# Kernel tuning notes

Hardware: AMD Instinct MI355X
Metric: run time of the kernel (lower is better)

The kernel has to match this reference:

```python
import jax, jax.numpy as jnp
import numpy as np

NUM_HEADS = 16
HEAD_DIM = 128
Q_SCALE = 0.05
Q_ZP = 8.0


def _quant_dequant_int4(x, scale, zp):
    # simulate int4 pack/unpack: q = clamp(round(x/scale + zp), 0, 15); deq = (q - zp) * scale
    qv = jnp.clip(jnp.round(x / scale + zp), 0.0, 15.0)
    return (qv - zp) * scale


def setup_inputs() -> dict:
    key = jax.random.key(0)
    kq, kk, kv = jax.random.split(key, 3)
    B, Sq, Sk, D = 4, 2048, 2048, 2048
    q = jax.random.normal(kq, (B, Sq, D), dtype=jnp.float32)
    k = jax.random.normal(kk, (B, Sk, D), dtype=jnp.float32)
    v = jax.random.normal(kv, (B, Sk, D), dtype=jnp.float32)
    mask = jnp.ones((B, Sk), dtype=bool)
    return {"q": q, "k": k, "v": v, "mask": mask, "q_start": 1000000000}


def reference(q, k, v, mask, q_start):
    B, Sq, d_model = q.shape
    Sk = k.shape[1]
    H, Dh = NUM_HEADS, HEAD_DIM
    # [B, H, S, Dh]
    qh = q.reshape(B, Sq, H, Dh).transpose(0, 2, 1, 3)
    kh = k.reshape(B, Sk, H, Dh).transpose(0, 2, 1, 3)
    vh = v.reshape(B, Sk, H, Dh).transpose(0, 2, 1, 3)
    # int4 quant-dequant of K and V (per-tensor scale/zero-point path)
    kd = _quant_dequant_int4(kh, Q_SCALE, Q_ZP)
    vd = _quant_dequant_int4(vh, Q_SCALE, Q_ZP)
    inv_sqrt_d = 1.0 / np.sqrt(Dh).astype(np.float32)
    scores = jnp.einsum('bhmd,bhnd->bhmn', qh, kd) * inv_sqrt_d  # [B,H,Sq,Sk]
    neg_inf = jnp.finfo(scores.dtype).min
    # key padding mask [B, Sk]
    scores = jnp.where(mask[:, None, None, :], scores, neg_inf)
    # causal mask with absolute query offset q_start (disabled when q_start is huge)
    m_abs = q_start + jnp.arange(Sq)[:, None]  # absolute query positions
    n_pos = jnp.arange(Sk)[None, :]
    scores = jnp.where(n_pos <= m_abs, scores, neg_inf)
    attn = jax.nn.softmax(scores, axis=-1)
    out = jnp.einsum('bhmn,bhnd->bhmd', attn, vd)  # [B,H,Sq,Dh]
    return out.transpose(0, 2, 1, 3).reshape(B, Sq, d_model)
```

## Files before the change

### kernel.cpp

```cpp
#include <hip/hip_runtime.h>


typedef __attribute__((ext_vector_type(8))) short short8;
typedef __attribute__((ext_vector_type(16))) float f32x16;

#define DEVI __device__ __forceinline__

namespace {

constexpr int DM = 2048;
constexpr int SQ = 2048;
constexpr int SK = 2048;
constexpr int DH = 128;
constexpr int KVB = 32;
constexpr int NT = SK / KVB;
constexpr int TILE_E = KVB * DH;
constexpr float CEXP = 0.12752051393f;

union US8 { unsigned short u[8]; short8 v; };
union UP4 { unsigned int u[4]; short8 v; };

DEVI unsigned short f2bf(float f) {
  unsigned int u = __float_as_uint(f);
  return (unsigned short)((u + 0x7fffu + ((u >> 16) & 1u)) >> 16);
}

DEVI float dq(float x) {
  float t = __builtin_rintf(__builtin_fmaf(x, 20.0f, 8.0f));
  t = __builtin_fmaxf(t, 0.0f);
  t = __builtin_fminf(t, 15.0f);
  return (t - 8.0f) * 0.05f;
}

DEVI unsigned short dqb(float x) { return f2bf(dq(x)); }

}

__global__ __launch_bounds__(512)
void eit3_pre(const float* __restrict__ kg, const float* __restrict__ vg,
              unsigned short* __restrict__ kws, unsigned short* __restrict__ vws)
{
  const int tid = threadIdx.x;
  const int t = blockIdx.x, h = blockIdx.y, b = blockIdx.z;
  const size_t tb = (((size_t)(b * 16 + h)) * NT + t) * TILE_E;
  __shared__ __align__(16) unsigned short KL[32 * 136];
  __shared__ __align__(16) unsigned short VL[32 * 136];

  {
    const int r = tid >> 4, c8 = (tid & 15) * 8;
    const float* ks = kg + ((size_t)b * SK + (size_t)t * KVB + r) * DM + h * DH + c8;
    const float* vs = vg + ((size_t)b * SK + (size_t)t * KVB + r) * DM + h * DH + c8;
    float4 ka = *(const float4*)ks, kb4 = *(const float4*)(ks + 4);
    float4 va = *(const float4*)vs, vb4 = *(const float4*)(vs + 4);
    US8 ok, ov;
    ok.u[0] = dqb(ka.x); ok.u[1] = dqb(ka.y); ok.u[2] = dqb(ka.z); ok.u[3] = dqb(ka.w);
    ok.u[4] = dqb(kb4.x); ok.u[5] = dqb(kb4.y); ok.u[6] = dqb(kb4.z); ok.u[7] = dqb(kb4.w);
    ov.u[0] = dqb(va.x); ov.u[1] = dqb(va.y); ov.u[2] = dqb(va.z); ov.u[3] = dqb(va.w);
    ov.u[4] = dqb(vb4.x); ov.u[5] = dqb(vb4.y); ov.u[6] = dqb(vb4.z); ov.u[7] = dqb(vb4.w);
    *(short8*)(KL + r * 136 + c8) = ok.v;
    *(short8*)(VL + r * 136 + c8) = ov.v;
  }
  __syncthreads();

  const int l = tid & 63;
  const int lq = l & 31, lh = (l >> 5) * 8;
  {
    const int s = tid >> 6;
    short8 o = *(const short8*)(KL + lq * 136 + s * 16 + lh);
    *(short8*)(kws + tb + (size_t)tid * 8) = o;
  }
  {
    const int f = tid >> 6, n = f >> 1, ks2 = f & 1;
    US8 o;
#pragma unroll
    for (int j = 0; j < 8; ++j)
      o.u[j] = VL[(ks2 * 16 + lh + j) * 136 + n * 32 + lq];
    *(short8*)(vws + tb + (size_t)tid * 8) = o.v;
  }
}

__global__ __launch_bounds__(64, 3)
void eit3_attn(const unsigned short* __restrict__ kws,
               const unsigned short* __restrict__ vws,
               const float* __restrict__ qg,
               const unsigned char* __restrict__ maskg,
               const int* __restrict__ qsg, float* __restrict__ outg)
{
  const int lane = threadIdx.x;
  const int hi   = lane >> 5;
  const int ql   = lane & 31;
  const int hi8  = hi * 8;
  const int phys = blockIdx.x;
  const int xcd = phys & 7, slot = phys >> 3;
  const int bh  = 8 * (slot >> 6) + xcd;
  const int sub = slot & 63;
  const int q0  = (sub >> 2) * 128 + (sub & 3) * 32;
  const int h = bh & 15, b = bh >> 4;
  const long long qstart = (long long)qsg[0];

  const unsigned char* mrow = maskg + (size_t)b * SK;
  int ok_u8 = 1, ok_i32 = 1;
  {
    const unsigned int* p = (const unsigned int*)(mrow + lane * 32);
#pragma unroll
    for (int j = 0; j < 8; ++j) {
      unsigned int x = p[j];
      int a = (x & 0xFFu) && (x & 0xFF00u) && (x & 0xFF0000u) && (x & 0xFF000000u);
      ok_u8 &= a;
      ok_i32 &= (x == 1u);
    }
  }
  const bool mask_all = __all(ok_u8) || __all(ok_i32);

  const size_t tbase = (size_t)bh * NT * TILE_E;
  const unsigned short* kb = kws + tbase + lane * 8;
  const unsigned short* vb = vws + tbase + lane * 8;

  short8 qf[8];
  {
    const float* qp = qg + ((size_t)b * SQ + q0 + ql) * DM + h * DH + hi8;
#pragma unroll
    for (int s = 0; s < 8; ++s) {
      float4 fa = *(const float4*)(qp + s * 16);
      float4 fb = *(const float4*)(qp + s * 16 + 4);
      US8 t;
      t.u[0] = f2bf(fa.x * CEXP); t.u[1] = f2bf(fa.y * CEXP);
      t.u[2] = f2bf(fa.z * CEXP); t.u[3] = f2bf(fa.w * CEXP);
      t.u[4] = f2bf(fb.x * CEXP); t.u[5] = f2bf(fb.y * CEXP);
      t.u[6] = f2bf(fb.z * CEXP); t.u[7] = f2bf(fb.w * CEXP);
      qf[s] = t.v;
    }
  }

  f32x16 zv;
#pragma unroll
  for (int r = 0; r < 16; ++r) zv[r] = 0.0f;
  f32x16 acc[4];
  acc[0] = zv; acc[1] = zv; acc[2] = zv; acc[3] = zv;
  float L = 0.0f;
  const long long qlim = qstart + (long long)(q0 + ql);

  for (int t = 0; t < NT; ++t) {
    const int kv0 = t * KVB;

    short8 kv[8];
    {
      const unsigned short* p = kb + (size_t)t * TILE_E;
#pragma unroll
      for (int s = 0; s < 8; ++s) kv[s] = *(const short8*)(p + s * 512);
    }

    f32x16 st = zv;
    __builtin_amdgcn_s_setprio(1);
#pragma unroll
    for (int s = 0; s < 8; ++s)
      st = __builtin_amdgcn_mfma_f32_32x32x16_bf16(kv[s], qf[s], st, 0, 0, 0);
    __builtin_amdgcn_s_setprio(0);

    {
      const unsigned short* p = vb + (size_t)t * TILE_E;
#pragma unroll
      for (int f = 0; f < 8; ++f) kv[f] = *(const short8*)(p + f * 512);
    }

    const bool fast = mask_all && ((long long)(kv0 + KVB - 1) <= qstart + (long long)q0);

    if (!fast) {
#pragma unroll
      for (int r = 0; r < 16; ++r) {
        int nl = (r & 3) + 8 * (r >> 2) + 4 * hi;
        bool ok = (mrow[kv0 + nl] != 0) && ((long long)(kv0 + nl) <= qlim);
        if (!ok) st[r] = -3.0e38f;
      }
    }

#pragma unroll
    for (int r = 0; r < 16; ++r)
      st[r] = __builtin_amdgcn_exp2f(st[r]);

    float s8[8];
#pragma unroll
    for (int i = 0; i < 8; ++i) s8[i] = st[i] + st[i + 8];
#pragma unroll
    for (int i = 0; i < 4; ++i) s8[i] = s8[i] + s8[i + 4];
    float ps = (s8[0] + s8[1]) + (s8[2] + s8[3]);
    ps += __shfl_xor(ps, 32);
    L += ps;

    short8 pa[2];
#pragma unroll
    for (int ks = 0; ks < 2; ++ks) {
      const int m8 = ks * 8;
      unsigned int X0, X1, Y0, Y1;
      asm("v_cvt_pk_bf16_f32 %0, %1, %2" : "=v"(X0) : "v"(st[m8 + 0]), "v"(st[m8 + 1]));
      asm("v_cvt_pk_bf16_f32 %0, %1, %2" : "=v"(X1) : "v"(st[m8 + 2]), "v"(st[m8 + 3]));
      asm("v_cvt_pk_bf16_f32 %0, %1, %2" : "=v"(Y0) : "v"(st[m8 + 4]), "v"(st[m8 + 5]));
      asm("v_cvt_pk_bf16_f32 %0, %1, %2" : "=v"(Y1) : "v"(st[m8 + 6]), "v"(st[m8 + 7]));
      asm("v_permlane32_swap_b32 %0, %1" : "+v"(X0), "+v"(Y0));
      asm("v_permlane32_swap_b32 %0, %1" : "+v"(X1), "+v"(Y1));
      UP4 P;
      P.u[0] = X0; P.u[1] = X1; P.u[2] = Y0; P.u[3] = Y1;
      pa[ks] = P.v;
    }

    __builtin_amdgcn_s_setprio(1);
#pragma unroll
    for (int n = 0; n < 4; ++n) {
#pragma unroll
      for (int ks = 0; ks < 2; ++ks)
        acc[n] = __builtin_amdgcn_mfma_f32_32x32x16_bf16(pa[ks], kv[n * 2 + ks],
                                                         acc[n], 0, 0, 0);
    }
    __builtin_amdgcn_s_setprio(0);
  }

  if (L == 0.0f) L = 1.0f;
  float rinv = 1.0f / L;
#pragma unroll
  for (int r = 0; r < 16; ++r) {
    int cr = (r & 3) + 8 * (r >> 2) + 4 * hi;
    float inv = __shfl(rinv, cr);
    float* op = outg + ((size_t)b * SQ + q0 + cr) * DM + h * DH + ql;
    op[0]  = acc[0][r] * inv;
    op[32] = acc[1][r] * inv;
    op[64] = acc[2][r] * inv;
    op[96] = acc[3][r] * inv;
  }
}

__global__ __launch_bounds__(512, 2)
void eit3_attn_fb(const float* __restrict__ qg, const float* __restrict__ kg,
                  const float* __restrict__ vg, const unsigned char* __restrict__ maskg,
                  const int* __restrict__ qsg, float* __restrict__ outg)
{
  const int tid  = threadIdx.x;
  const int lane = tid & 63;
  const int w    = tid >> 6;
  const int hi   = lane >> 5;
  const int ql   = lane & 31;
  const int qb = blockIdx.x;
  const int h  = blockIdx.y;
  const int b  = blockIdx.z;
  const int q0 = qb * 256;
  const long long qstart = (long long)qsg[0];

  __shared__ __align__(16) unsigned short Ksh[64 * 128];
  __shared__ __align__(16) unsigned short Vsh[64 * 128];
  __shared__ unsigned char mskSh[64];

  const unsigned int vbase = (unsigned int)(size_t)(void*)Vsh;

  const unsigned char* mrow = maskg + (size_t)b * SK;
  int ok_u8, ok_i32;
  {
    const unsigned char* p4 = mrow + tid * 4;
    unsigned char b0 = p4[0], b1 = p4[1], b2 = p4[2], b3 = p4[3];
    ok_u8  = (b0 && b1 && b2 && b3);
    ok_i32 = (b0 && !b1 && !b2 && !b3);
  }
  const int a_u8  = __syncthreads_and(ok_u8);
  const int a_i32 = __syncthreads_and(ok_i32);
  const bool mask_all = (a_u8 | a_i32) != 0;

  short8 qf[8];
  {
    const int qrow = q0 + w * 32 + ql;
    const float* qp = qg + ((size_t)b * SQ + qrow) * DM + h * DH + hi * 8;
#pragma unroll
    for (int s = 0; s < 8; ++s) {
      float4 fa = *(const float4*)(qp + s * 16);
      float4 fb = *(const float4*)(qp + s * 16 + 4);
      US8 t;
      t.u[0] = f2bf(fa.x); t.u[1] = f2bf(fa.y); t.u[2] = f2bf(fa.z); t.u[3] = f2bf(fa.w);
      t.u[4] = f2bf(fb.x); t.u[5] = f2bf(fb.y); t.u[6] = f2bf(fb.z); t.u[7] = f2bf(fb.w);
      qf[s] = t.v;
    }
  }

  f32x16 zv;
#pragma unroll
  for (int r = 0; r < 16; ++r) zv[r] = 0.0f;
  f32x16 acc[4];
  acc[0] = zv; acc[1] = zv; acc[2] = zv; acc[3] = zv;
  float M = -3.0e38f, L = 0.0f;

  const float* kptr = kg + ((size_t)b * SK) * DM + h * DH;
  const float* vptr = vg + ((size_t)b * SK) * DM + h * DH;

  constexpr float CEXP2 = 0.12752051393f;
  for (int kv0 = 0; kv0 < SK; kv0 += 64) {
    __syncthreads();
#pragma unroll
    for (int j = 0; j < 2; ++j) {
      int idx = tid + 512 * j;
      int n = idx >> 4, d8 = idx & 15;
      const float* gp = kptr + (size_t)(kv0 + n) * DM + d8 * 8;
      float4 fa = *(const float4*)gp;
      float4 fb = *(const float4*)(gp + 4);
      US8 t;
      t.u[0] = dqb(fa.x); t.u[1] = dqb(fa.y); t.u[2] = dqb(fa.z); t.u[3] = dqb(fa.w);
      t.u[4] = dqb(fb.x); t.u[5] = dqb(fb.y); t.u[6] = dqb(fb.z); t.u[7] = dqb(fb.w);
      int ui = (n * 128 + d8 * 8) ^ ((n & 7) << 3);
      *(short8*)(Ksh + ui) = t.v;
    }
    {
      int kr = w * 8 + (lane & 7);
      int c3 = lane >> 3;
#pragma unroll
      for (int j = 0; j < 4; ++j) {
        int d4 = c3 + 8 * j;
        const float* gp = vptr + (size_t)(kv0 + kr) * DM + d4 * 4;
        float4 fa = *(const float4*)gp;
        ushort4 tv;
        tv.x = dqb(fa.x); tv.y = dqb(fa.y); tv.z = dqb(fa.z); tv.w = dqb(fa.w);
        int d = d4 * 4;
        int ui = ((kr >> 2) * 8 + (d >> 4)) * 64 + (kr & 3) * 16 + (d & 15);
        *(ushort4*)(Vsh + ui) = tv;
      }
    }
    const bool causal_ok = ((long long)kv0 + 63) <= (qstart + (long long)q0);
    const bool fast = mask_all && causal_ok;
    if (!fast && w == 0) mskSh[lane] = mrow[kv0 + lane];
    __syncthreads();

    f32x16 st[2];
#pragma unroll
    for (int t = 0; t < 2; ++t) {
      f32x16 sa = zv;
#pragma unroll
      for (int s = 0; s < 8; ++s) {
        int kr = t * 32 + ql;
        int ui = (kr * 128 + s * 16 + hi * 8) ^ ((kr & 7) << 3);
        short8 af = *(const short8*)(Ksh + ui);
        sa = __builtin_amdgcn_mfma_f32_32x32x16_bf16(af, qf[s], sa, 0, 0, 0);
      }
      st[t] = sa;
    }
    if (!fast) {
      const long long qlim = qstart + (long long)(q0 + w * 32 + ql);
#pragma unroll
      for (int t = 0; t < 2; ++t) {
#pragma unroll
        for (int r = 0; r < 16; ++r) {
          int nl = t * 32 + (r & 3) + 8 * (r >> 2) + 4 * hi;
          bool ok = (mskSh[nl] != 0) && ((long long)(kv0 + nl) <= qlim);
          if (!ok) st[t][r] = -3.0e38f;
        }
      }
    }
    f32x16 red;
#pragma unroll
    for (int r = 0; r < 16; ++r) red[r] = __builtin_fmaxf(st[0][r], st[1][r]);
#pragma unroll
    for (int r = 0; r < 8; ++r) red[r] = __builtin_fmaxf(red[r], red[r + 8]);
#pragma unroll
    for (int r = 0; r < 4; ++r) red[r] = __builtin_fmaxf(red[r], red[r + 4]);
    float pmax = __builtin_fmaxf(__builtin_fmaxf(red[0], red[1]),
                                 __builtin_fmaxf(red[2], red[3]));
    pmax = __builtin_fmaxf(pmax, __shfl_xor(pmax, 32));
    const float Mnew = __builtin_fmaxf(M, pmax);
    const float scale = __builtin_amdgcn_exp2f((M - Mnew) * CEXP2);
#pragma unroll
    for (int t = 0; t < 2; ++t) {
#pragma unroll
      for (int r = 0; r < 16; ++r)
        st[t][r] = __builtin_amdgcn_exp2f((st[t][r] - Mnew) * CEXP2);
    }
    if (!fast) {
      const long long qlim = qstart + (long long)(q0 + w * 32 + ql);
#pragma unroll
      for (int t = 0; t < 2; ++t) {
#pragma unroll
        for (int r = 0; r < 16; ++r) {
          int nl = t * 32 + (r & 3) + 8 * (r >> 2) + 4 * hi;
          bool ok = (mskSh[nl] != 0) && ((long long)(kv0 + nl) <= qlim);
          if (!ok) st[t][r] = 0.0f;
        }
      }
    }
    f32x16 sx;
#pragma unroll
    for (int r = 0; r < 16; ++r) sx[r] = st[0][r] + st[1][r];
#pragma unroll
    for (int r = 0; r < 8; ++r) sx[r] = sx[r] + sx[r + 8];
#pragma unroll
    for (int r = 0; r < 4; ++r) sx[r] = sx[r] + sx[r + 4];
    float ps = (sx[0] + sx[1]) + (sx[2] + sx[3]);
    ps += __shfl_xor(ps, 32);
    L = L * scale + ps;
    if (!__all(Mnew == M)) {
#pragma unroll
      for (int r = 0; r < 16; ++r) {
        float sc = __shfl(scale, (r & 3) + 8 * (r >> 2) + 4 * hi);
        acc[0][r] *= sc; acc[1][r] *= sc; acc[2][r] *= sc; acc[3][r] *= sc;
      }
    }
    M = Mnew;

    short8 pa[4];
#pragma unroll
    for (int ks = 0; ks < 4; ++ks) {
      const int t = ks >> 1;
      const int m8 = (ks & 1) * 8;
      unsigned int X0, X1, Y0, Y1;
      asm("v_cvt_pk_bf16_f32 %0, %1, %2" : "=v"(X0) : "v"(st[t][m8 + 0]), "v"(st[t][m8 + 1]));
      asm("v_cvt_pk_bf16_f32 %0, %1, %2" : "=v"(X1) : "v"(st[t][m8 + 2]), "v"(st[t][m8 + 3]));
      asm("v_cvt_pk_bf16_f32 %0, %1, %2" : "=v"(Y0) : "v"(st[t][m8 + 4]), "v"(st[t][m8 + 5]));
      asm("v_cvt_pk_bf16_f32 %0, %1, %2" : "=v"(Y1) : "v"(st[t][m8 + 6]), "v"(st[t][m8 + 7]));
      asm("v_permlane32_swap_b32 %0, %1" : "+v"(X0), "+v"(Y0));
      asm("v_permlane32_swap_b32 %0, %1" : "+v"(X1), "+v"(Y1));
      UP4 P;
      P.u[0] = X0; P.u[1] = X1; P.u[2] = Y0; P.u[3] = Y1;
      pa[ks] = P.v;
    }
#pragma unroll
    for (int n = 0; n < 4; ++n) {
      unsigned long long t0[4], t1[4];
#pragma unroll
      for (int ks = 0; ks < 4; ++ks) {
        unsigned int addr = vbase
          + (unsigned int)(((4 * ks + 2 * hi) * 8 + 2 * n + ((lane >> 4) & 1)) * 128)
          + (unsigned int)((lane & 15) * 8);
        asm volatile("ds_read_b64_tr_b16 %0, %1" : "=v"(t0[ks]) : "v"(addr));
        asm volatile("ds_read_b64_tr_b16 %0, %1 offset:1024" : "=v"(t1[ks]) : "v"(addr));
      }
      asm volatile("s_waitcnt lgkmcnt(0)" ::: "memory");
      __builtin_amdgcn_sched_barrier(0);
#pragma unroll
      for (int ks = 0; ks < 4; ++ks) {
        union { unsigned long long q[2]; short8 v; } vb2;
        vb2.q[0] = t0[ks]; vb2.q[1] = t1[ks];
        acc[n] = __builtin_amdgcn_mfma_f32_32x32x16_bf16(pa[ks], vb2.v, acc[n], 0, 0, 0);
      }
    }
  }

  if (L == 0.0f) L = 1.0f;
  float rinv = 1.0f / L;
#pragma unroll
  for (int r = 0; r < 16; ++r) {
    int cr = (r & 3) + 8 * (r >> 2) + 4 * hi;
    float inv = __shfl(rinv, cr);
    float* op = outg + ((size_t)b * SQ + (q0 + w * 32 + cr)) * DM + h * DH + ql;
    op[0]  = acc[0][r] * inv;
    op[32] = acc[1][r] * inv;
    op[64] = acc[2][r] * inv;
    op[96] = acc[3][r] * inv;
  }
}

extern "C" void kernel_launch(void* const* d_in, const int* in_sizes, int n_in,
                              void* d_out, int out_size, void* d_ws, size_t ws_size,
                              hipStream_t stream) {
  (void)in_sizes; (void)n_in; (void)out_size;
  const float* q = (const float*)d_in[0];
  const float* k = (const float*)d_in[1];
  const float* v = (const float*)d_in[2];
  const unsigned char* mask = (const unsigned char*)d_in[3];
  const int* qs = (const int*)d_in[4];

  const size_t need = (size_t)2 * 16777216 * 2;
  if (ws_size >= need) {
    unsigned short* kws = (unsigned short*)d_ws;
    unsigned short* vws = kws + 16777216;
    dim3 pgrid(NT, 16, 4);
    eit3_pre<<<pgrid, dim3(512), 0, stream>>>(k, v, kws, vws);
    eit3_attn<<<dim3(4096), dim3(64), 0, stream>>>(kws, vws, q, mask, qs, (float*)d_out);
  } else {
    dim3 grid(SQ / 256, 16, 4);
    eit3_attn_fb<<<grid, dim3(512), 0, stream>>>(q, k, v, mask, qs, (float*)d_out);
  }
}
```

Before: 216.4 us.

## Process two query tiles per wave and double-buffer K/V register loads

Each single-wave block now handles 64 query rows (two 32-row tiles) instead of 32, so every K and V fragment loaded is reused for twice as many MFMAs, and the grid is halved. K/V fragments for the next tile are prefetched into a second register set while the current tile computes. This roughly doubles accumulator and fragment register use and drops the occupancy hint, which may lower waves per SIMD and reduce latency hiding.

```diff
diff --git a/kernel.cpp b/kernel.cpp
--- a/kernel.cpp
+++ b/kernel.cpp
@@ -79,7 +79,7 @@
   }
 }
 
-__global__ __launch_bounds__(64, 3)
+__global__ __launch_bounds__(64)
 void eit3_attn(const unsigned short* __restrict__ kws,
                const unsigned short* __restrict__ vws,
                const float* __restrict__ qg,
@@ -92,9 +92,8 @@
   const int hi8  = hi * 8;
   const int phys = blockIdx.x;
   const int xcd = phys & 7, slot = phys >> 3;
-  const int bh  = 8 * (slot >> 6) + xcd;
-  const int sub = slot & 63;
-  const int q0  = (sub >> 2) * 128 + (sub & 3) * 32;
+  const int bh  = 8 * (slot >> 5) + xcd;
+  const int q0  = (slot & 31) * 64;
   const int h = bh & 15, b = bh >> 4;
   const long long qstart = (long long)qsg[0];
 
@@ -116,52 +115,66 @@
   const unsigned short* kb = kws + tbase + lane * 8;
   const unsigned short* vb = vws + tbase + lane * 8;
 
-  short8 qf[8];
+  short8 qf0[8], qf1[8];
   {
     const float* qp = qg + ((size_t)b * SQ + q0 + ql) * DM + h * DH + hi8;
 #pragma unroll
     for (int s = 0; s < 8; ++s) {
-      float4 fa = *(const float4*)(qp + s * 16);
-      float4 fb = *(const float4*)(qp + s * 16 + 4);
-      US8 t;
-      t.u[0] = f2bf(fa.x * CEXP); t.u[1] = f2bf(fa.y * CEXP);
-      t.u[2] = f2bf(fa.z * CEXP); t.u[3] = f2bf(fa.w * CEXP);
-      t.u[4] = f2bf(fb.x * CEXP); t.u[5] = f2bf(fb.y * CEXP);
-      t.u[6] = f2bf(fb.z * CEXP); t.u[7] = f2bf(fb.w * CEXP);
-      qf[s] = t.v;
+      float4 a0 = *(const float4*)(qp + s * 16);
+      float4 c0 = *(const float4*)(qp + s * 16 + 4);
+      float4 a1 = *(const float4*)(qp + 32 * DM + s * 16);
+      float4 c1 = *(const float4*)(qp + 32 * DM + s * 16 + 4);
+      US8 t0, t1;
+      t0.u[0] = f2bf(a0.x * CEXP); t0.u[1] = f2bf(a0.y * CEXP);
+      t0.u[2] = f2bf(a0.z * CEXP); t0.u[3] = f2bf(a0.w * CEXP);
+      t0.u[4] = f2bf(c0.x * CEXP); t0.u[5] = f2bf(c0.y * CEXP);
+      t0.u[6] = f2bf(c0.z * CEXP); t0.u[7] = f2bf(c0.w * CEXP);
+      t1.u[0] = f2bf(a1.x * CEXP); t1.u[1] = f2bf(a1.y * CEXP);
+      t1.u[2] = f2bf(a1.z * CEXP); t1.u[3] = f2bf(a1.w * CEXP);
+      t1.u[4] = f2bf(c1.x * CEXP); t1.u[5] = f2bf(c1.y * CEXP);
+      t1.u[6] = f2bf(c1.z * CEXP); t1.u[7] = f2bf(c1.w * CEXP);
+      qf0[s] = t0.v; qf1[s] = t1.v;
     }
   }
 
   f32x16 zv;
 #pragma unroll
   for (int r = 0; r < 16; ++r) zv[r] = 0.0f;
-  f32x16 acc[4];
-  acc[0] = zv; acc[1] = zv; acc[2] = zv; acc[3] = zv;
-  float L = 0.0f;
-  const long long qlim = qstart + (long long)(q0 + ql);
-
-  for (int t = 0; t < NT; ++t) {
+  f32x16 acc0[4], acc1[4];
+#pragma unroll
+  for (int n = 0; n < 4; ++n) { acc0[n] = zv; acc1[n] = zv; }
+  float L0 = 0.0f, L1 = 0.0f;
+  const long long qlim0 = qstart + (long long)(q0 + ql);
+
+  short8 kfA[8], vfA[8], kfB[8], vfB[8];
+  {
+#pragma unroll
+    for (int s = 0; s < 8; ++s) kfA[s] = *(const short8*)(kb + s * 512);
+#pragma unroll
+    for (int s = 0; s < 8; ++s) vfA[s] = *(const short8*)(vb + s * 512);
+  }
+
+  auto step = [&](int t, short8 (&kfP)[8], short8 (&vfP)[8],
+                  short8 (&kfN)[8], short8 (&vfN)[8]) {
     const int kv0 = t * KVB;
-
-    short8 kv[8];
     {
-      const unsigned short* p = kb + (size_t)t * TILE_E;
-#pragma unroll
-      for (int s = 0; s < 8; ++s) kv[s] = *(const short8*)(p + s * 512);
-    }
-
-    f32x16 st = zv;
+      const int tn = (t + 1 < NT) ? (t + 1) : (NT - 1);
+      const unsigned short* pk = kb + (size_t)tn * TILE_E;
+      const unsigned short* pv = vb + (size_t)tn * TILE_E;
+#pragma unroll
+      for (int s = 0; s < 8; ++s) kfN[s] = *(const short8*)(pk + s * 512);
+#pragma unroll
+      for (int s = 0; s < 8; ++s) vfN[s] = *(const short8*)(pv + s * 512);
+    }
+
+    f32x16 st0 = zv, st1 = zv;
     __builtin_amdgcn_s_setprio(1);
 #pragma unroll
-    for (int s = 0; s < 8; ++s)
-      st = __builtin_amdgcn_mfma_f32_32x32x16_bf16(kv[s], qf[s], st, 0, 0, 0);
+    for (int s = 0; s < 8; ++s) {
+      st0 = __builtin_amdgcn_mfma_f32_32x32x16_bf16(kfP[s], qf0[s], st0, 0, 0, 0);
+      st1 = __builtin_amdgcn_mfma_f32_32x32x16_bf16(kfP[s], qf1[s], st1, 0, 0, 0);
+    }
     __builtin_amdgcn_s_setprio(0);
-
-    {
-      const unsigned short* p = vb + (size_t)t * TILE_E;
-#pragma unroll
-      for (int f = 0; f < 8; ++f) kv[f] = *(const short8*)(p + f * 512);
-    }
 
     const bool fast = mask_all && ((long long)(kv0 + KVB - 1) <= qstart + (long long)q0);
 
@@ -169,62 +182,88 @@
 #pragma unroll
       for (int r = 0; r < 16; ++r) {
         int nl = (r & 3) + 8 * (r >> 2) + 4 * hi;
-        bool ok = (mrow[kv0 + nl] != 0) && ((long long)(kv0 + nl) <= qlim);
-        if (!ok) st[r] = -3.0e38f;
-      }
-    }
-
-#pragma unroll
-    for (int r = 0; r < 16; ++r)
-      st[r] = __builtin_amdgcn_exp2f(st[r]);
-
-    float s8[8];
-#pragma unroll
-    for (int i = 0; i < 8; ++i) s8[i] = st[i] + st[i + 8];
-#pragma unroll
-    for (int i = 0; i < 4; ++i) s8[i] = s8[i] + s8[i + 4];
-    float ps = (s8[0] + s8[1]) + (s8[2] + s8[3]);
-    ps += __shfl_xor(ps, 32);
-    L += ps;
-
-    short8 pa[2];
-#pragma unroll
-    for (int ks = 0; ks < 2; ++ks) {
-      const int m8 = ks * 8;
-      unsigned int X0, X1, Y0, Y1;
-      asm("v_cvt_pk_bf16_f32 %0, %1, %2" : "=v"(X0) : "v"(st[m8 + 0]), "v"(st[m8 + 1]));
-      asm("v_cvt_pk_bf16_f32 %0, %1, %2" : "=v"(X1) : "v"(st[m8 + 2]), "v"(st[m8 + 3]));
-      asm("v_cvt_pk_bf16_f32 %0, %1, %2" : "=v"(Y0) : "v"(st[m8 + 4]), "v"(st[m8 + 5]));
-      asm("v_cvt_pk_bf16_f32 %0, %1, %2" : "=v"(Y1) : "v"(st[m8 + 6]), "v"(st[m8 + 7]));
-      asm("v_permlane32_swap_b32 %0, %1" : "+v"(X0), "+v"(Y0));
-      asm("v_permlane32_swap_b32 %0, %1" : "+v"(X1), "+v"(Y1));
-      UP4 P;
-      P.u[0] = X0; P.u[1] = X1; P.u[2] = Y0; P.u[3] = Y1;
-      pa[ks] = P.v;
+        bool okm = (mrow[kv0 + nl] != 0);
+        bool ok0 = okm && ((long long)(kv0 + nl) <= qlim0);
+        bool ok1 = okm && ((long long)(kv0 + nl) <= qlim0 + 32);
+        if (!ok0) st0[r] = -3.0e38f;
+        if (!ok1) st1[r] = -3.0e38f;
+      }
+    }
+
+#pragma unroll
+    for (int r = 0; r < 16; ++r) {
+      st0[r] = __builtin_amdgcn_exp2f(st0[r]);
+      st1[r] = __builtin_amdgcn_exp2f(st1[r]);
+    }
+
+    float s80[8], s81[8];
+#pragma unroll
+    for (int i = 0; i < 8; ++i) { s80[i] = st0[i] + st0[i + 8]; s81[i] = st1[i] + st1[i + 8]; }
+#pragma unroll
+    for (int i = 0; i < 4; ++i) { s80[i] = s80[i] + s80[i + 4]; s81[i] = s81[i] + s81[i + 4]; }
+    float p0 = (s80[0] + s80[1]) + (s80[2] + s80[3]);
+    float p1 = (s81[0] + s81[1]) + (s81[2] + s81[3]);
+    p0 += __shfl_xor(p0, 32);
+    p1 += __shfl_xor(p1, 32);
+    L0 += p0; L1 += p1;
+
+    short8 pa0[2], pa1[2];
+#pragma unroll
+    for (int half = 0; half < 2; ++half) {
+      const f32x16& sth = half ? st1 : st0;
+      short8* pah = half ? pa1 : pa0;
+#pragma unroll
+      for (int ks = 0; ks < 2; ++ks) {
+        const int m8 = ks * 8;
+        unsigned int X0, X1, Y0, Y1;
+        asm("v_cvt_pk_bf16_f32 %0, %1, %2" : "=v"(X0) : "v"(sth[m8 + 0]), "v"(sth[m8 + 1]));
+        asm("v_cvt_pk_bf16_f32 %0, %1, %2" : "=v"(X1) : "v"(sth[m8 + 2]), "v"(sth[m8 + 3]));
+        asm("v_cvt_pk_bf16_f32 %0, %1, %2" : "=v"(Y0) : "v"(sth[m8 + 4]), "v"(sth[m8 + 5]));
+        asm("v_cvt_pk_bf16_f32 %0, %1, %2" : "=v"(Y1) : "v"(sth[m8 + 6]), "v"(sth[m8 + 7]));
+        asm("v_permlane32_swap_b32 %0, %1" : "+v"(X0), "+v"(Y0));
+        asm("v_permlane32_swap_b32 %0, %1" : "+v"(X1), "+v"(Y1));
+        UP4 P;
+        P.u[0] = X0; P.u[1] = X1; P.u[2] = Y0; P.u[3] = Y1;
+        pah[ks] = P.v;
+      }
     }
 
     __builtin_amdgcn_s_setprio(1);
 #pragma unroll
     for (int n = 0; n < 4; ++n) {
 #pragma unroll
-      for (int ks = 0; ks < 2; ++ks)
-        acc[n] = __builtin_amdgcn_mfma_f32_32x32x16_bf16(pa[ks], kv[n * 2 + ks],
-                                                         acc[n], 0, 0, 0);
+      for (int ks = 0; ks < 2; ++ks) {
+        acc0[n] = __builtin_amdgcn_mfma_f32_32x32x16_bf16(pa0[ks], vfP[n * 2 + ks],
+                                                          acc0[n], 0, 0, 0);
+        acc1[n] = __builtin_amdgcn_mfma_f32_32x32x16_bf16(pa1[ks], vfP[n * 2 + ks],
+                                                          acc1[n], 0, 0, 0);
+      }
     }
     __builtin_amdgcn_s_setprio(0);
-  }
-
-  if (L == 0.0f) L = 1.0f;
-  float rinv = 1.0f / L;
+  };
+
+  for (int t = 0; t < NT; t += 2) {
+    step(t,     kfA, vfA, kfB, vfB);
+    step(t + 1, kfB, vfB, kfA, vfA);
+  }
+
+  if (L0 == 0.0f) L0 = 1.0f;
+  if (L1 == 0.0f) L1 = 1.0f;
+  float ri0 = 1.0f / L0, ri1 = 1.0f / L1;
 #pragma unroll
   for (int r = 0; r < 16; ++r) {
     int cr = (r & 3) + 8 * (r >> 2) + 4 * hi;
-    float inv = __shfl(rinv, cr);
-    float* op = outg + ((size_t)b * SQ + q0 + cr) * DM + h * DH + ql;
-    op[0]  = acc[0][r] * inv;
-    op[32] = acc[1][r] * inv;
-    op[64] = acc[2][r] * inv;
-    op[96] = acc[3][r] * inv;
+    float i0 = __shfl(ri0, cr), i1 = __shfl(ri1, cr);
+    float* op0 = outg + ((size_t)b * SQ + q0 + cr) * DM + h * DH + ql;
+    float* op1 = op0 + 32 * DM;
+    op0[0]  = acc0[0][r] * i0;
+    op0[32] = acc0[1][r] * i0;
+    op0[64] = acc0[2][r] * i0;
+    op0[96] = acc0[3][r] * i0;
+    op1[0]  = acc1[0][r] * i1;
+    op1[32] = acc1[1][r] * i1;
+    op1[64] = acc1[2][r] * i1;
+    op1[96] = acc1[3][r] * i1;
   }
 }
 
@@ -465,7 +504,7 @@
     unsigned short* vws = kws + 16777216;
     dim3 pgrid(NT, 16, 4);
     eit3_pre<<<pgrid, dim3(512), 0, stream>>>(k, v, kws, vws);
-    eit3_attn<<<dim3(4096), dim3(64), 0, stream>>>(kws, vws, q, mask, qs, (float*)d_out);
+    eit3_attn<<<dim3(2048), dim3(64), 0, stream>>>(kws, vws, q, mask, qs, (float*)d_out);
   } else {
     dim3 grid(SQ / 256, 16, 4);
     eit3_attn_fb<<<grid, dim3(512), 0, stream>>>(q, k, v, mask, qs, (float*)d_out);
```

After: 197.9 us (median of 2 runs). 1.09x faster.
